# Optimization experiments

Measured on AMD Instinct MI355X. Metric: run time of the kernel, lower is better.

## Reference

```python
import jax, jax.numpy as jnp
import numpy as np

HEADS, BATCH, SEQ, CDIM = 8, 4, 2048, 32
WINDOW = 10

def setup_inputs() -> dict:
    key = jax.random.key(0)
    k1, k2, k3, k4 = jax.random.split(key, 4)
    shp = (HEADS, BATCH, SEQ, CDIM)
    return {
        'Q': jax.random.normal(k1, shp, dtype=jnp.float32),
        'K': jax.random.normal(k2, shp, dtype=jnp.float32),
        'V': jax.random.normal(k3, shp, dtype=jnp.float32),
        'G': jax.random.normal(k4, shp, dtype=jnp.float32),
        'seqMask': jnp.zeros((BATCH, SEQ), dtype=bool),  # no padded positions
    }

def reference(Q, K, V, G, seqMask):
    # Q,K,V,G: [h, n, s, c]; seqMask: [n, s] bool (True = masked key position)
    scale = 1.0 / jnp.sqrt(jnp.asarray(CDIM, dtype=Q.dtype))
    A = jnp.einsum('hnsi,hnti->hnst', Q, K) * scale  # [h,n,s,t]
    # padding mask on key axis
    A = jnp.where(seqMask[None, :, None, :], -jnp.inf, A)
    # local band mask |s-t| <= WINDOW (torch scatter construction clamps to
    # row bounds, which is equivalent to the plain band)
    idx = jnp.arange(SEQ)
    band = jnp.abs(idx[:, None] - idx[None, :]) <= WINDOW  # [s,t]
    A = jnp.where(band[None, None, :, :], A, -jnp.inf)
    A = jax.nn.softmax(A, axis=-1)
    # gated AV fusion: out[n,s,h,i] = sum_t A[h,n,s,t] V[h,n,t,i] * G[h,n,s,i]
    out = jnp.einsum('hnst,hnti,hnsi->nshi', A, V, G)
    return out
```

## Files before the change

### kernel.cpp

```cpp
#include <hip/hip_runtime.h>
#include <hip/hip_bf16.h>
#include <math.h>

#define HEADS 8
#define BATCH 4
#define SEQ 2048
#define CDIM 32
#define WINDOW 10

#define RPB 64
#define VROWS 96
#define VSTR 20

typedef float f32x4 __attribute__((ext_vector_type(4)));
typedef short s16x8 __attribute__((ext_vector_type(8)));
#define MFMA16 __builtin_amdgcn_mfma_f32_16x16x32_bf16

union BF8 { s16x8 v; __hip_bfloat162 h[4]; };
union U32 { __hip_bfloat162 h; unsigned u; };
union U4  { unsigned u[4]; s16x8 v; };

__global__ __launch_bounds__(256) void lwin_attn_kernel(
    const float* __restrict__ Q, const float* __restrict__ K,
    const float* __restrict__ V, const float* __restrict__ G,
    const unsigned char* __restrict__ seqMask, float* __restrict__ out)
{
    __shared__ unsigned V_s[VROWS * VSTR];

    const int d = blockIdx.x;
    const int b = (d & 7) * 128 + (d >> 3);

    const int hn = b >> 5;
    const int s0 = (b & 31) * RPB;
    const int n  = hn & 3;
    const int h  = hn >> 2;
    const int base_hn = hn * SEQ * CDIM;

    const int tid  = threadIdx.x;
    const int w    = tid >> 6;
    const int lane = tid & 63;
    const int q    = lane & 15;
    const int g    = lane >> 4;

    {
        const int i = tid >> 2, o = tid & 3;
        const int t  = s0 - 16 + i;
        const int tc = min(max(t, 0), SEQ - 1);
        const float4 f0 = *(const float4*)&V[base_hn + tc * 32 + 4 * o];
        const float4 f1 = *(const float4*)&V[base_hn + tc * 32 + 16 + 4 * o];
        U32 w0, w1, w2, w3;
        w0.h = __float22bfloat162_rn(make_float2(f0.x, f1.x));
        w1.h = __float22bfloat162_rn(make_float2(f0.y, f1.y));
        w2.h = __float22bfloat162_rn(make_float2(f0.z, f1.z));
        w3.h = __float22bfloat162_rn(make_float2(f0.w, f1.w));
        *(uint4*)&V_s[i * VSTR + 4 * o] = make_uint4(w0.u, w1.u, w2.u, w3.u);
    }
    if (tid < 128) {
        const int task = tid + 256;
        const int i = task >> 2, o = task & 3;
        const int t  = s0 - 16 + i;
        const int tc = min(max(t, 0), SEQ - 1);
        const float4 f0 = *(const float4*)&V[base_hn + tc * 32 + 4 * o];
        const float4 f1 = *(const float4*)&V[base_hn + tc * 32 + 16 + 4 * o];
        U32 w0, w1, w2, w3;
        w0.h = __float22bfloat162_rn(make_float2(f0.x, f1.x));
        w1.h = __float22bfloat162_rn(make_float2(f0.y, f1.y));
        w2.h = __float22bfloat162_rn(make_float2(f0.z, f1.z));
        w3.h = __float22bfloat162_rn(make_float2(f0.w, f1.w));
        *(uint4*)&V_s[i * VSTR + 4 * o] = make_uint4(w0.u, w1.u, w2.u, w3.u);
    }

    const int sw = s0 + 16 * w;

    const int rowq = hn * SEQ + sw + q;
    const float sc = 0.17677669529663687f * 1.4426950408889634f;
    const float4 q0 = *(const float4*)&Q[rowq * 32 + 8 * g];
    const float4 q1 = *(const float4*)&Q[rowq * 32 + 8 * g + 4];
    BF8 bq;
    bq.h[0] = __float22bfloat162_rn(make_float2(q0.x * sc, q0.y * sc));
    bq.h[1] = __float22bfloat162_rn(make_float2(q0.z * sc, q0.w * sc));
    bq.h[2] = __float22bfloat162_rn(make_float2(q1.x * sc, q1.y * sc));
    bq.h[3] = __float22bfloat162_rn(make_float2(q1.z * sc, q1.w * sc));
    const float4 g0 = *(const float4*)&G[rowq * 32 + 4 * g];
    const float4 g1 = *(const float4*)&G[rowq * 32 + 16 + 4 * g];

    BF8 ak[3];
#pragma unroll
    for (int blk = 0; blk < 3; ++blk) {
        const int t  = sw - 16 + 16 * blk + q;
        const int tc = min(max(t, 0), SEQ - 1);
        const float4 k0 = *(const float4*)&K[base_hn + tc * 32 + 8 * g];
        const float4 k1 = *(const float4*)&K[base_hn + tc * 32 + 8 * g + 4];
        ak[blk].h[0] = __float22bfloat162_rn(make_float2(k0.x, k0.y));
        ak[blk].h[1] = __float22bfloat162_rn(make_float2(k0.z, k0.w));
        ak[blk].h[2] = __float22bfloat162_rn(make_float2(k1.x, k1.y));
        ak[blk].h[3] = __float22bfloat162_rn(make_float2(k1.z, k1.w));
    }

    unsigned long long mI;
    {
        const int t  = sw - 16 + lane;
        const int tc = min(max(t, 0), SEQ - 1);
        const bool inval = (t < 0) || (t >= SEQ) || (seqMask[n * SEQ + tc] != 0);
        mI = __ballot(inval);
    }
    const unsigned long long vm = (0x1FFFFFULL << (q + 6)) & ~mI;

    f32x4 S[3];
#pragma unroll
    for (int blk = 0; blk < 3; ++blk)
        S[blk] = MFMA16(ak[blk].v, bq.v, (f32x4){0.f, 0.f, 0.f, 0.f}, 0, 0, 0);

    float sm = 0.f;
    unsigned pk[3][2];
#pragma unroll
    for (int blk = 0; blk < 3; ++blk) {
        float e[4];
#pragma unroll
        for (int r = 0; r < 4; ++r) {
            const int j = 16 * blk + 4 * g + r;
            const float x = ((vm >> j) & 1ULL) ? S[blk][r] : -1e30f;
            e[r] = __builtin_amdgcn_exp2f(x);
            sm += e[r];
        }
        U32 a, b2;
        a.h  = __float22bfloat162_rn(make_float2(e[0], e[1]));
        b2.h = __float22bfloat162_rn(make_float2(e[2], e[3]));
        pk[blk][0] = a.u;
        pk[blk][1] = b2.u;
    }
    sm += __shfl_xor(sm, 16);
    sm += __shfl_xor(sm, 32);

    __syncthreads();

    f32x4 O0 = {0.f, 0.f, 0.f, 0.f}, O1 = {0.f, 0.f, 0.f, 0.f};
    {
        const int R = 16 * w;
        unsigned r0[4], r1[4];
#pragma unroll
        for (int jj = 0; jj < 4; ++jj) {
            r0[jj] = V_s[(R + 4 * g + jj) * VSTR + q];
            r1[jj] = V_s[(R + 16 + 4 * g + jj) * VSTR + q];
        }
        U4 A0, A1v;
        A0.u[0]  = __builtin_amdgcn_perm(r0[1], r0[0], 0x05040100u);
        A0.u[1]  = __builtin_amdgcn_perm(r0[3], r0[2], 0x05040100u);
        A0.u[2]  = __builtin_amdgcn_perm(r1[1], r1[0], 0x05040100u);
        A0.u[3]  = __builtin_amdgcn_perm(r1[3], r1[2], 0x05040100u);
        A1v.u[0] = __builtin_amdgcn_perm(r0[1], r0[0], 0x07060302u);
        A1v.u[1] = __builtin_amdgcn_perm(r0[3], r0[2], 0x07060302u);
        A1v.u[2] = __builtin_amdgcn_perm(r1[1], r1[0], 0x07060302u);
        A1v.u[3] = __builtin_amdgcn_perm(r1[3], r1[2], 0x07060302u);
        U4 Bp;
        Bp.u[0] = pk[0][0]; Bp.u[1] = pk[0][1];
        Bp.u[2] = pk[1][0]; Bp.u[3] = pk[1][1];
        O0 = MFMA16(A0.v,  Bp.v, O0, 0, 0, 0);
        O1 = MFMA16(A1v.v, Bp.v, O1, 0, 0, 0);
    }
    {
        const int R = 16 * w + 32;
        unsigned r0[4];
#pragma unroll
        for (int jj = 0; jj < 4; ++jj)
            r0[jj] = V_s[(R + 4 * g + jj) * VSTR + q];
        U4 A0, A1v;
        A0.u[0]  = __builtin_amdgcn_perm(r0[1], r0[0], 0x05040100u);
        A0.u[1]  = __builtin_amdgcn_perm(r0[3], r0[2], 0x05040100u);
        A0.u[2]  = 0u; A0.u[3] = 0u;
        A1v.u[0] = __builtin_amdgcn_perm(r0[1], r0[0], 0x07060302u);
        A1v.u[1] = __builtin_amdgcn_perm(r0[3], r0[2], 0x07060302u);
        A1v.u[2] = 0u; A1v.u[3] = 0u;
        U4 Bp;
        Bp.u[0] = pk[2][0]; Bp.u[1] = pk[2][1];
        Bp.u[2] = 0u;       Bp.u[3] = 0u;
        O0 = MFMA16(A0.v,  Bp.v, O0, 0, 0, 0);
        O1 = MFMA16(A1v.v, Bp.v, O1, 0, 0, 0);
    }

    const float invq = 1.0f / sm;
    float4 o0, o1;
    o0.x = O0[0] * invq * g0.x;  o0.y = O0[1] * invq * g0.y;
    o0.z = O0[2] * invq * g0.z;  o0.w = O0[3] * invq * g0.w;
    o1.x = O1[0] * invq * g1.x;  o1.y = O1[1] * invq * g1.y;
    o1.z = O1[2] * invq * g1.z;  o1.w = O1[3] * invq * g1.w;
    float* obase = &out[((n * SEQ + sw + q) * HEADS + h) * 32];
    *(float4*)&obase[4 * g]      = o0;
    *(float4*)&obase[16 + 4 * g] = o1;
}

extern "C" void kernel_launch(void* const* d_in, const int* in_sizes, int n_in,
                              void* d_out, int out_size, void* d_ws, size_t ws_size,
                              hipStream_t stream) {
    const float* Q = (const float*)d_in[0];
    const float* K = (const float*)d_in[1];
    const float* V = (const float*)d_in[2];
    const float* G = (const float*)d_in[3];
    const unsigned char* seqMask = (const unsigned char*)d_in[4];
    float* out = (float*)d_out;

    const int blocks = HEADS * BATCH * (SEQ / RPB);
    lwin_attn_kernel<<<blocks, 256, 0, stream>>>(Q, K, V, G, seqMask, out);
}
```

Before: 14.17 us.

## Stage K tile in shared memory and trim halo loads to the needed rows

K rows are now cooperatively loaded once per block, converted to bf16 and stored in shared memory, instead of each wave loading its own overlapping 48 K rows from global memory. V and K staging now loads only rows 6..89 of the 96-row halo, and the unused edge rows of V_s are zero-filled. The barrier moves before the QK MFMA, which adds LDS traffic and a sync point earlier in the kernel in exchange for fewer redundant global loads.

```diff
diff --git a/kernel.cpp b/kernel.cpp
--- a/kernel.cpp
+++ b/kernel.cpp
@@ -25,6 +25,7 @@
     const float* __restrict__ V, const float* __restrict__ G,
     const unsigned char* __restrict__ seqMask, float* __restrict__ out)
 {
+    __shared__ short    K_s[VROWS * 32];
     __shared__ unsigned V_s[VROWS * VSTR];
 
     const int d = blockIdx.x;
@@ -42,37 +43,45 @@
     const int q    = lane & 15;
     const int g    = lane >> 4;
 
-    {
-        const int i = tid >> 2, o = tid & 3;
-        const int t  = s0 - 16 + i;
-        const int tc = min(max(t, 0), SEQ - 1);
-        const float4 f0 = *(const float4*)&V[base_hn + tc * 32 + 4 * o];
-        const float4 f1 = *(const float4*)&V[base_hn + tc * 32 + 16 + 4 * o];
-        U32 w0, w1, w2, w3;
-        w0.h = __float22bfloat162_rn(make_float2(f0.x, f1.x));
-        w1.h = __float22bfloat162_rn(make_float2(f0.y, f1.y));
-        w2.h = __float22bfloat162_rn(make_float2(f0.z, f1.z));
-        w3.h = __float22bfloat162_rn(make_float2(f0.w, f1.w));
-        *(uint4*)&V_s[i * VSTR + 4 * o] = make_uint4(w0.u, w1.u, w2.u, w3.u);
-    }
-    if (tid < 128) {
-        const int task = tid + 256;
-        const int i = task >> 2, o = task & 3;
-        const int t  = s0 - 16 + i;
-        const int tc = min(max(t, 0), SEQ - 1);
-        const float4 f0 = *(const float4*)&V[base_hn + tc * 32 + 4 * o];
-        const float4 f1 = *(const float4*)&V[base_hn + tc * 32 + 16 + 4 * o];
-        U32 w0, w1, w2, w3;
-        w0.h = __float22bfloat162_rn(make_float2(f0.x, f1.x));
-        w1.h = __float22bfloat162_rn(make_float2(f0.y, f1.y));
-        w2.h = __float22bfloat162_rn(make_float2(f0.z, f1.z));
-        w3.h = __float22bfloat162_rn(make_float2(f0.w, f1.w));
-        *(uint4*)&V_s[i * VSTR + 4 * o] = make_uint4(w0.u, w1.u, w2.u, w3.u);
-    }
-
-    const int sw = s0 + 16 * w;
-
+#pragma unroll
+    for (int it = 0; it < 3; ++it) {
+        const int task = tid + it * 256;
+        if (task < 336) {
+            const int i = 6 + (task >> 2), o = task & 3;
+            const int t  = s0 - 16 + i;
+            const int tc = min(max(t, 0), SEQ - 1);
+            const float4 f0 = *(const float4*)&K[base_hn + tc * 32 + 8 * o];
+            const float4 f1 = *(const float4*)&K[base_hn + tc * 32 + 8 * o + 4];
+            BF8 u;
+            u.h[0] = __float22bfloat162_rn(make_float2(f0.x, f0.y));
+            u.h[1] = __float22bfloat162_rn(make_float2(f0.z, f0.w));
+            u.h[2] = __float22bfloat162_rn(make_float2(f1.x, f1.y));
+            u.h[3] = __float22bfloat162_rn(make_float2(f1.z, f1.w));
+            *(s16x8*)&K_s[i * 32 + 8 * o] = u.v;
+        } else if (task < 672) {
+            const int vt = task - 336;
+            const int i = 6 + (vt >> 2), o = vt & 3;
+            const int t  = s0 - 16 + i;
+            const int tc = min(max(t, 0), SEQ - 1);
+            const float4 f0 = *(const float4*)&V[base_hn + tc * 32 + 4 * o];
+            const float4 f1 = *(const float4*)&V[base_hn + tc * 32 + 16 + 4 * o];
+            U32 w0, w1, w2, w3;
+            w0.h = __float22bfloat162_rn(make_float2(f0.x, f1.x));
+            w1.h = __float22bfloat162_rn(make_float2(f0.y, f1.y));
+            w2.h = __float22bfloat162_rn(make_float2(f0.z, f1.z));
+            w3.h = __float22bfloat162_rn(make_float2(f0.w, f1.w));
+            *(uint4*)&V_s[i * VSTR + 4 * o] = make_uint4(w0.u, w1.u, w2.u, w3.u);
+        } else if (task < 720) {
+            const int zt = task - 672;
+            const int zr = zt >> 2, o = zt & 3;
+            const int i = (zr < 6) ? zr : 84 + zr;
+            *(uint4*)&V_s[i * VSTR + 4 * o] = make_uint4(0u, 0u, 0u, 0u);
+        }
+    }
+
+    const int sw   = s0 + 16 * w;
     const int rowq = hn * SEQ + sw + q;
+
     const float sc = 0.17677669529663687f * 1.4426950408889634f;
     const float4 q0 = *(const float4*)&Q[rowq * 32 + 8 * g];
     const float4 q1 = *(const float4*)&Q[rowq * 32 + 8 * g + 4];
@@ -81,21 +90,8 @@
     bq.h[1] = __float22bfloat162_rn(make_float2(q0.z * sc, q0.w * sc));
     bq.h[2] = __float22bfloat162_rn(make_float2(q1.x * sc, q1.y * sc));
     bq.h[3] = __float22bfloat162_rn(make_float2(q1.z * sc, q1.w * sc));
-    const float4 g0 = *(const float4*)&G[rowq * 32 + 4 * g];
-    const float4 g1 = *(const float4*)&G[rowq * 32 + 16 + 4 * g];
-
-    BF8 ak[3];
-#pragma unroll
-    for (int blk = 0; blk < 3; ++blk) {
-        const int t  = sw - 16 + 16 * blk + q;
-        const int tc = min(max(t, 0), SEQ - 1);
-        const float4 k0 = *(const float4*)&K[base_hn + tc * 32 + 8 * g];
-        const float4 k1 = *(const float4*)&K[base_hn + tc * 32 + 8 * g + 4];
-        ak[blk].h[0] = __float22bfloat162_rn(make_float2(k0.x, k0.y));
-        ak[blk].h[1] = __float22bfloat162_rn(make_float2(k0.z, k0.w));
-        ak[blk].h[2] = __float22bfloat162_rn(make_float2(k1.x, k1.y));
-        ak[blk].h[3] = __float22bfloat162_rn(make_float2(k1.z, k1.w));
-    }
+    const float4 ga = *(const float4*)&G[rowq * 32 + 4 * g];
+    const float4 gb = *(const float4*)&G[rowq * 32 + 16 + 4 * g];
 
     unsigned long long mI;
     {
@@ -106,10 +102,14 @@
     }
     const unsigned long long vm = (0x1FFFFFULL << (q + 6)) & ~mI;
 
+    __syncthreads();
+
     f32x4 S[3];
 #pragma unroll
-    for (int blk = 0; blk < 3; ++blk)
-        S[blk] = MFMA16(ak[blk].v, bq.v, (f32x4){0.f, 0.f, 0.f, 0.f}, 0, 0, 0);
+    for (int blk = 0; blk < 3; ++blk) {
+        const s16x8 ak = *(const s16x8*)&K_s[(16 * w + 16 * blk + q) * 32 + 8 * g];
+        S[blk] = MFMA16(ak, bq.v, (f32x4){0.f, 0.f, 0.f, 0.f}, 0, 0, 0);
+    }
 
     float sm = 0.f;
     unsigned pk[3][2];
@@ -131,8 +131,6 @@
     }
     sm += __shfl_xor(sm, 16);
     sm += __shfl_xor(sm, 32);
-
-    __syncthreads();
 
     f32x4 O0 = {0.f, 0.f, 0.f, 0.f}, O1 = {0.f, 0.f, 0.f, 0.f};
     {
@@ -180,10 +178,10 @@
 
     const float invq = 1.0f / sm;
     float4 o0, o1;
-    o0.x = O0[0] * invq * g0.x;  o0.y = O0[1] * invq * g0.y;
-    o0.z = O0[2] * invq * g0.z;  o0.w = O0[3] * invq * g0.w;
-    o1.x = O1[0] * invq * g1.x;  o1.y = O1[1] * invq * g1.y;
-    o1.z = O1[2] * invq * g1.z;  o1.w = O1[3] * invq * g1.w;
+    o0.x = O0[0] * invq * ga.x;  o0.y = O0[1] * invq * ga.y;
+    o0.z = O0[2] * invq * ga.z;  o0.w = O0[3] * invq * ga.w;
+    o1.x = O1[0] * invq * gb.x;  o1.y = O1[1] * invq * gb.y;
+    o1.z = O1[2] * invq * gb.z;  o1.w = O1[3] * invq * gb.w;
     float* obase = &out[((n * SEQ + sw + q) * HEADS + h) * 32];
     *(float4*)&obase[4 * g]      = o0;
     *(float4*)&obase[16 + 4 * g] = o1;
```

New measurement: 12.64 us. 10.8% less time.
